# Optimization experiments

Hardware: AMD Instinct MI355X
Metric: run time of the kernel (lower is better)

## Reference

```python
import jax, jax.numpy as jnp
import numpy as np

D_MODEL, D_STATE, D_CONV, EXPAND, HEADDIM = 256, 16, 4, 2, 16
D_INNER = EXPAND * D_MODEL            # 512
NHEADS = D_INNER // HEADDIM           # 32
CONV_DIM = D_INNER + 2 * D_STATE      # 544 (ngroups=1)
D_IN_PROJ = 2 * D_INNER + 2 * D_STATE + NHEADS  # 1088
BATCH, SEQLEN = 8, 4096


def setup_inputs() -> dict:
    key = jax.random.key(0)
    ks = jax.random.split(key, 8)
    u = jax.random.normal(ks[0], (BATCH, SEQLEN, D_MODEL), jnp.float32)
    W_in = jax.random.normal(ks[1], (D_MODEL, D_IN_PROJ), jnp.float32) * 0.02
    conv_w = jax.random.normal(ks[2], (CONV_DIM, 1, D_CONV), jnp.float32) * 0.2
    conv_b = jnp.zeros((CONV_DIM,), jnp.float32)
    # dt_bias init: inverse-softplus of dt ~ Uniform in log-space [dt_min, dt_max]
    dt = jnp.exp(jax.random.uniform(ks[3], (NHEADS,), jnp.float32)
                 * (np.log(0.1) - np.log(0.001)) + np.log(0.001))
    dt = jnp.clip(dt, 1e-4, None)
    dt_bias = dt + jnp.log(-jnp.expm1(-dt))
    A_log = jnp.log(jax.random.uniform(ks[4], (NHEADS,), jnp.float32, 1.0, 16.0))
    D = jnp.ones((NHEADS,), jnp.float32)
    norm_w = jnp.ones((D_INNER,), jnp.float32)
    W_out = jax.random.normal(ks[5], (D_INNER, D_MODEL), jnp.float32) * 0.02
    return dict(u=u, W_in=W_in, conv_w=conv_w, conv_b=conv_b, dt_bias=dt_bias,
                A_log=A_log, D=D, norm_w=norm_w, W_out=W_out)


def _mamba2_forward(u, W_in, conv_w, conv_b, dt_bias, A_log, D, norm_w, W_out):
    batch, seqlen, _ = u.shape
    zxbcdt = u @ W_in                                   # (B, L, 2*d_inner + 2*N + H)
    z = zxbcdt[..., :D_INNER]                           # gate
    xBC = zxbcdt[..., D_INNER:2 * D_INNER + 2 * D_STATE]
    dt = jax.nn.softplus(zxbcdt[..., -NHEADS:] + dt_bias)  # (B, L, H)
    # causal depthwise conv1d over time + SiLU
    xc = jnp.transpose(xBC, (0, 2, 1))                  # (B, C, L)
    xc = jax.lax.conv_general_dilated(
        xc, conv_w, window_strides=(1,), padding=[(D_CONV - 1, 0)],
        feature_group_count=CONV_DIM, dimension_numbers=('NCH', 'OIH', 'NCH'))
    xBC = jax.nn.silu(jnp.transpose(xc, (0, 2, 1)) + conv_b)
    x = xBC[..., :D_INNER].reshape(batch, seqlen, NHEADS, HEADDIM)  # (B,L,H,P)
    Bm = xBC[..., D_INNER:D_INNER + D_STATE]            # (B, L, N), ngroups=1
    Cm = xBC[..., D_INNER + D_STATE:]                   # (B, L, N)
    A = -jnp.exp(A_log)                                 # (H,)
    dA = jnp.exp(dt * A)                                # (B, L, H) decay per step

    # selective scan: h_t = dA_t * h_{t-1} + dt_t * (B_t outer x_t); y_t = C_t . h_t
    def step(h, inp):
        da_t, dt_t, b_t, x_t, c_t = inp
        h = da_t[:, :, None, None] * h + jnp.einsum('bh,bn,bhp->bhpn', dt_t, b_t, x_t)
        y_t = jnp.einsum('bhpn,bn->bhp', h, c_t)
        return h, y_t

    h0 = jnp.zeros((batch, NHEADS, HEADDIM, D_STATE), u.dtype)
    xs = (jnp.moveaxis(dA, 1, 0), jnp.moveaxis(dt, 1, 0),
          jnp.moveaxis(Bm, 1, 0), jnp.moveaxis(x, 1, 0), jnp.moveaxis(Cm, 1, 0))
    _, ys = jax.lax.scan(step, h0, xs)                  # ys: (L, B, H, P)
    y = jnp.moveaxis(ys, 0, 1) + D[None, None, :, None] * x
    y = y.reshape(batch, seqlen, D_INNER)
    # gated RMSNorm (norm_before_gate=False): normalize(y * silu(z)) * weight
    t = y * jax.nn.silu(z)
    t = t * jax.lax.rsqrt(jnp.mean(t * t, axis=-1, keepdims=True) + 1e-5) * norm_w
    return t @ W_out


def reference(u, W_in, conv_w, conv_b, dt_bias, A_log, D, norm_w, W_out):
    return _mamba2_forward(u, W_in, conv_w, conv_b, dt_bias, A_log, D, norm_w, W_out)
```

## Files before the change

### kernel.cpp

```cpp
#include <hip/hip_runtime.h>
#include <hip/hip_bf16.h>
#include <math.h>

#define BATCH   8
#define SEQLEN  4096
#define DMODEL  256
#define DSTATE  16
#define NHEADS  32
#define HEADDIM 16
#define DINNER  512
#define CONVDIM 544
#define DINPROJ 1088
#define NROWS   (BATCH*SEQLEN)
#define CHUNK   64
#define NCH     (SEQLEN/CHUNK)

typedef __attribute__((ext_vector_type(8))) short short8;
typedef __attribute__((ext_vector_type(8))) unsigned short ushort8;
typedef __attribute__((ext_vector_type(4))) float f32x4;

#define LDSP(x) ((__attribute__((address_space(3))) void*)(x))
#define GLBP(x) ((const __attribute__((address_space(1))) void*)(x))

__device__ __forceinline__ float bfu2f(unsigned short u){
  union { float f; unsigned int i; } x; x.i = ((unsigned int)u) << 16; return x.f;
}
__device__ __forceinline__ unsigned short f2bfu(float f){
  union { float f; unsigned int u; } v; v.f = f;
  v.u += 0x7fffu + ((v.u >> 16) & 1u);
  return (unsigned short)(v.u >> 16);
}

__global__ __launch_bounds__(256) void k_cast_u(const float* __restrict__ u, unsigned short* __restrict__ ub){
  int i = blockIdx.x*256 + threadIdx.x;
  float4 v = reinterpret_cast<const float4*>(u)[i];
  ushort4 o; o.x=f2bfu(v.x); o.y=f2bfu(v.y); o.z=f2bfu(v.z); o.w=f2bfu(v.w);
  reinterpret_cast<ushort4*>(ub)[i] = o;
}

__global__ __launch_bounds__(256) void k_transpose_cast(const float* __restrict__ W, unsigned short* __restrict__ WT, int K, int N){
  int idx = blockIdx.x*256 + threadIdx.x;
  if (idx >= N*K) return;
  int n = idx / K, k = idx - n*K;
  WT[idx] = f2bfu(W[(size_t)k*N + n]);
}

template<int EPI, int BN>
__global__ __launch_bounds__(256) void k_gemm(
    const unsigned short* __restrict__ A,
    const unsigned short* __restrict__ BT,
    int K, int nbase,
    unsigned short* __restrict__ oz,
    unsigned short* __restrict__ oxbc,
    float* __restrict__ odtraw,
    float* __restrict__ of32, int Nout)
{
  constexpr int ABYTES = 128*64;
  constexpr int BBYTES = BN*64;
  constexpr int BUFB   = ABYTES + BBYTES;
  constexpr int NF     = BN/32;
  constexpr int BCALLS = BBYTES/4096;
  __shared__ __align__(16) unsigned char lds[2*BUFB];
  const int tid = threadIdx.x;
  const int l   = tid & 63;
  const int w   = tid >> 6;
  const int wr  = w >> 1, wc = w & 1;
  const int bm0 = blockIdx.x * 128;
  const int bn0 = nbase + blockIdx.y * BN;
  const int fr  = l & 15, kq = l >> 4;
  f32x4 acc[4][NF] = {};

  auto STAGE = [&](int buf, int kt){
    const int k0 = kt << 5;
    unsigned char* lb = (unsigned char*)lds + buf*BUFB;
    #pragma unroll
    for (int i = 0; i < 2; ++i){
      int row = w*32 + i*16 + (l>>2);
      int sl  = (l&3) ^ ((row>>1)&3);
      const unsigned short* gp = A + (size_t)(bm0+row)*K + k0 + sl*8;
      __builtin_amdgcn_global_load_lds(GLBP(gp), LDSP(lb + w*2048 + i*1024), 16, 0, 0);
    }
    #pragma unroll
    for (int i = 0; i < BCALLS; ++i){
      int row = w*(BCALLS*16) + i*16 + (l>>2);
      int sl  = (l&3) ^ ((row>>1)&3);
      const unsigned short* gp = BT + (size_t)(bn0+row)*K + k0 + sl*8;
      __builtin_amdgcn_global_load_lds(GLBP(gp), LDSP(lb + ABYTES + w*(BCALLS*1024) + i*1024), 16, 0, 0);
    }
  };

  const int nK = K >> 5;
  STAGE(0, 0);
  __syncthreads();
  int cur = 0;
  for (int kt = 0; kt < nK; ++kt){
    if (kt + 1 < nK) STAGE(cur^1, kt+1);
    const unsigned char* ab = (const unsigned char*)lds + cur*BUFB;
    const unsigned char* bb = ab + ABYTES;
    short8 bf[NF];
    #pragma unroll
    for (int nf = 0; nf < NF; ++nf){
      int rb = wc*(BN/2) + nf*16 + fr;
      bf[nf] = *reinterpret_cast<const short8*>(bb + rb*64 + ((kq ^ ((rb>>1)&3))*16));
    }
    #pragma unroll
    for (int mf = 0; mf < 4; ++mf){
      int ra = wr*64 + mf*16 + fr;
      short8 af = *reinterpret_cast<const short8*>(ab + ra*64 + ((kq ^ ((ra>>1)&3))*16));
      #pragma unroll
      for (int nf = 0; nf < NF; ++nf)
        acc[mf][nf] = __builtin_amdgcn_mfma_f32_16x16x32_bf16(af, bf[nf], acc[mf][nf], 0, 0, 0);
    }
    __syncthreads();
    cur ^= 1;
  }
  #pragma unroll
  for (int mf = 0; mf < 4; ++mf){
    #pragma unroll
    for (int nf = 0; nf < NF; ++nf){
      #pragma unroll
      for (int r = 0; r < 4; ++r){
        int m = bm0 + wr*64 + mf*16 + kq*4 + r;
        int n = bn0 + wc*(BN/2) + nf*16 + fr;
        float v = acc[mf][nf][r];
        if (EPI == 1){
          if (n < DINNER)                 oz[(size_t)m*DINNER + n] = f2bfu(v);
          else if (n < DINNER + CONVDIM)  oxbc[(size_t)m*CONVDIM + (n - DINNER)] = f2bfu(v);
          else                            odtraw[(size_t)m*NHEADS + (n - DINNER - CONVDIM)] = v;
        } else {
          of32[(size_t)m*Nout + n] = v;
        }
      }
    }
  }
}

__global__ __launch_bounds__(256) void k_convbc(const unsigned short* __restrict__ xbc,
                                                const float* __restrict__ cw,
                                                const float* __restrict__ cb,
                                                float* __restrict__ bco){
  const int tid = threadIdx.x;
  const int j = tid & 31;
  const int rt = tid >> 5;
  const int r0 = blockIdx.x*64 + rt*8;
  const int ch = 512 + j;
  const int tloc = r0 & (SEQLEN-1);
  float wv0 = cw[ch*4+0], wv1 = cw[ch*4+1], wv2 = cw[ch*4+2], wv3 = cw[ch*4+3];
  const float bias = cb[ch];
  float xr[11];
  #pragma unroll
  for (int k = 0; k < 11; ++k){
    int r = r0 - 3 + k;
    xr[k] = (tloc - 3 + k < 0) ? 0.f : bfu2f(xbc[(size_t)r*CONVDIM + ch]);
  }
  #pragma unroll
  for (int i = 0; i < 8; ++i){
    float acc = fmaf(wv0, xr[i], fmaf(wv1, xr[i+1], fmaf(wv2, xr[i+2], fmaf(wv3, xr[i+3], bias))));
    bco[(size_t)(r0+i)*32 + j] = acc / (1.f + __expf(-acc));
  }
}

__global__ __launch_bounds__(256) void k_dtda(const float* __restrict__ dtraw,
                                              const float* __restrict__ dt_bias,
                                              const float* __restrict__ A_log,
                                              float* __restrict__ dt_o,
                                              float* __restrict__ dA_o){
  int i = blockIdx.x*256 + threadIdx.x;
  int h = i & (NHEADS-1);
  float x = dtraw[i] + dt_bias[h];
  float dt = (x > 20.f) ? x : log1pf(expf(x));
  dt_o[i] = dt;
  dA_o[i] = expf(-expf(A_log[h]) * dt);
}

__global__ __launch_bounds__(256,4) void k_scan1(
    const unsigned short* __restrict__ xbc, const float* __restrict__ bc,
    const float* __restrict__ dta, const float* __restrict__ daa,
    const float* __restrict__ cwv, const float* __restrict__ cbv,
    const float* __restrict__ Dv,
    float* __restrict__ yl, float* __restrict__ st, float* __restrict__ Pp)
{
  __shared__ float sBC[65*32];
  __shared__ float sdt[65*16];
  __shared__ float sda[65*16];
  const int tid = threadIdx.x;
  const int bid = blockIdx.x;
  const int qh = bid & 1;
  const int c  = (bid >> 1) & (NCH-1);
  const int b  = bid >> 7;
  const int w  = tid >> 6;
  const int l  = tid & 63;
  const int q  = qh*4 + w;
  const int hh = l >> 4, p = l & 15;
  const int h  = q*4 + hh;
  const size_t row0 = (size_t)b*SEQLEN + (size_t)c*CHUNK;
  const int xoff = q*64 + l;
  {
    const float* src = bc + row0*32;
    #pragma unroll
    for (int i = 0; i < 2; ++i){
      int idx = tid + i*256;
      *reinterpret_cast<float4*>(&sBC[idx*4]) = *reinterpret_cast<const float4*>(src + (size_t)idx*4);
    }
  }
  {
    int t = tid >> 2, g = (tid & 3)*4;
    *reinterpret_cast<float4*>(&sdt[t*16+g]) =
      *reinterpret_cast<const float4*>(dta + (row0+t)*NHEADS + qh*16 + g);
    *reinterpret_cast<float4*>(&sda[t*16+g]) =
      *reinterpret_cast<const float4*>(daa + (row0+t)*NHEADS + qh*16 + g);
  }
  const float cw0 = cwv[xoff*4+0], cw1 = cwv[xoff*4+1], cw2 = cwv[xoff*4+2], cw3 = cwv[xoff*4+3];
  const float cb0 = cbv[xoff];
  const float Dh = Dv[h];
  const int dIdx = w*4 + hh;
  float wA, wB, wC;
  if (c == 0){ wA = wB = wC = 0.f; }
  else {
    wA = bfu2f(xbc[(row0-3)*CONVDIM + xoff]);
    wB = bfu2f(xbc[(row0-2)*CONVDIM + xoff]);
    wC = bfu2f(xbc[(row0-1)*CONVDIM + xoff]);
  }
  float xq0 = bfu2f(xbc[(row0+0)*CONVDIM + xoff]);
  float xq1 = bfu2f(xbc[(row0+1)*CONVDIM + xoff]);
  float xq2 = bfu2f(xbc[(row0+2)*CONVDIM + xoff]);
  float xq3 = bfu2f(xbc[(row0+3)*CONVDIM + xoff]);
  __syncthreads();
  float BA[32], BB[32];
  #pragma unroll
  for (int k = 0; k < 8; ++k)
    *reinterpret_cast<float4*>(&BA[4*k]) = *reinterpret_cast<const float4*>(&sBC[4*k]);
  float dtA = sdt[dIdx], daA = sda[dIdx];
  float dtB, daB;
  float hs[16];
  #pragma unroll
  for (int n = 0; n < 16; ++n) hs[n] = 0.f;
  float cum = 1.f;

#define S1STEP(CUR, NXT, DTC, DAC, DTN, DAN, XQ, T) {                          \
    const int t_ = (T);                                                        \
    _Pragma("unroll")                                                          \
    for (int k = 0; k < 8; ++k)                                                \
      *reinterpret_cast<float4*>(&NXT[4*k]) =                                  \
        *reinterpret_cast<const float4*>(&sBC[(t_+1)*32 + 4*k]);               \
    DTN = sdt[(t_+1)*16 + dIdx]; DAN = sda[(t_+1)*16 + dIdx];                  \
    float xnew = bfu2f(xbc[(row0 + t_ + 4)*CONVDIM + xoff]);                   \
    float xc = fmaf(cw0, wA, fmaf(cw1, wB, fmaf(cw2, wC, fmaf(cw3, XQ, cb0))));\
    wA = wB; wB = wC; wC = XQ; XQ = xnew;                                      \
    float xs = xc / (1.f + __expf(-xc));                                       \
    float dx = DTC * xs;                                                       \
    float y_ = 0.f;                                                            \
    _Pragma("unroll")                                                          \
    for (int n = 0; n < 16; ++n) hs[n] = fmaf(DAC, hs[n], dx*CUR[n]);          \
    _Pragma("unroll")                                                          \
    for (int n = 0; n < 16; ++n) y_ = fmaf(hs[n], CUR[16+n], y_);              \
    cum *= DAC;                                                                \
    yl[(row0 + t_)*DINNER + xoff] = y_ + Dh*xs;                                \
  }

  for (int T = 0; T < CHUNK; T += 4){
    S1STEP(BA, BB, dtA, daA, dtB, daB, xq0, T+0);
    S1STEP(BB, BA, dtB, daB, dtA, daA, xq1, T+1);
    S1STEP(BA, BB, dtA, daA, dtB, daB, xq2, T+2);
    S1STEP(BB, BA, dtB, daB, dtA, daA, xq3, T+3);
  }
#undef S1STEP
  float* sp = st + (((size_t)(b*NHEADS + h)*NCH + c)*16 + p)*16;
  #pragma unroll
  for (int k = 0; k < 4; ++k)
    *reinterpret_cast<float4*>(sp + 4*k) = make_float4(hs[4*k], hs[4*k+1], hs[4*k+2], hs[4*k+3]);
  if (p == 0) Pp[((size_t)b*NHEADS + h)*NCH + c] = cum;
}

__global__ __launch_bounds__(64) void k_scan2(float* __restrict__ st, const float* __restrict__ Pp){
  const int bh = blockIdx.x;
  const int l = threadIdx.x;
  float* sb = st + (size_t)bh*NCH*256 + l*4;
  const float* pb = Pp + (size_t)bh*NCH;
  float4 carry = make_float4(0.f,0.f,0.f,0.f);
  float4 Hb[4]; float Pb[4];
  #pragma unroll
  for (int i = 0; i < 4; ++i){
    Hb[i] = *reinterpret_cast<const float4*>(sb + (size_t)i*256);
    Pb[i] = pb[i];
  }
  for (int c0 = 0; c0 < NCH; c0 += 4){
    #pragma unroll
    for (int i = 0; i < 4; ++i){
      const int cc = c0 + i;
      float4 Hc = Hb[i]; float Pc = Pb[i];
      if (cc + 4 < NCH){
        Hb[i] = *reinterpret_cast<const float4*>(sb + (size_t)(cc+4)*256);
        Pb[i] = pb[cc+4];
      }
      *reinterpret_cast<float4*>(sb + (size_t)cc*256) = carry;
      carry.x = fmaf(Pc, carry.x, Hc.x);
      carry.y = fmaf(Pc, carry.y, Hc.y);
      carry.z = fmaf(Pc, carry.z, Hc.z);
      carry.w = fmaf(Pc, carry.w, Hc.w);
    }
  }
}

__global__ __launch_bounds__(256,4) void k_scan3(
    const float* __restrict__ yl, const float* __restrict__ bc,
    const float* __restrict__ daa, const float* __restrict__ st,
    unsigned short* __restrict__ ybf)
{
  __shared__ float sC[65*16];
  __shared__ float sda[65*16];
  const int tid = threadIdx.x;
  const int bid = blockIdx.x;
  const int qh = bid & 1;
  const int c  = (bid >> 1) & (NCH-1);
  const int b  = bid >> 7;
  const int w  = tid >> 6;
  const int l  = tid & 63;
  const int q  = qh*4 + w;
  const int hh = l >> 4, p = l & 15;
  const int h  = q*4 + hh;
  const size_t row0 = (size_t)b*SEQLEN + (size_t)c*CHUNK;
  const int xoff = q*64 + l;
  {
    int t = tid >> 2, g = (tid & 3)*4;
    *reinterpret_cast<float4*>(&sC[t*16+g]) =
      *reinterpret_cast<const float4*>(bc + (row0+t)*32 + 16 + g);
    *reinterpret_cast<float4*>(&sda[t*16+g]) =
      *reinterpret_cast<const float4*>(daa + (row0+t)*NHEADS + qh*16 + g);
  }
  float hi[16];
  {
    const float* sp = st + (((size_t)(b*NHEADS + h)*NCH + c)*16 + p)*16;
    #pragma unroll
    for (int k = 0; k < 4; ++k){
      float4 v = *reinterpret_cast<const float4*>(sp + 4*k);
      hi[4*k] = v.x; hi[4*k+1] = v.y; hi[4*k+2] = v.z; hi[4*k+3] = v.w;
    }
  }
  float yq0 = yl[(row0+0)*DINNER + xoff];
  float yq1 = yl[(row0+1)*DINNER + xoff];
  float yq2 = yl[(row0+2)*DINNER + xoff];
  float yq3 = yl[(row0+3)*DINNER + xoff];
  __syncthreads();
  const int dIdx = w*4 + hh;
  float CA[16], CB[16];
  #pragma unroll
  for (int k = 0; k < 4; ++k)
    *reinterpret_cast<float4*>(&CA[4*k]) = *reinterpret_cast<const float4*>(&sC[4*k]);
  float daA = sda[dIdx], daB;
  float cum = 1.f;

#define S3STEP(CUR, NXT, DAC, DAN, YQ, T) {                                    \
    const int t_ = (T);                                                        \
    _Pragma("unroll")                                                          \
    for (int k = 0; k < 4; ++k)                                                \
      *reinterpret_cast<float4*>(&NXT[4*k]) =                                  \
        *reinterpret_cast<const float4*>(&sC[(t_+1)*16 + 4*k]);                \
    DAN = sda[(t_+1)*16 + dIdx];                                               \
    float ynew = yl[(row0 + t_ + 4)*DINNER + xoff];                            \
    cum *= DAC;                                                                \
    float corr = 0.f;                                                          \
    _Pragma("unroll")                                                          \
    for (int n = 0; n < 16; ++n) corr = fmaf(hi[n], CUR[n], corr);             \
    ybf[(row0 + t_)*DINNER + xoff] = f2bfu(YQ + cum*corr);                     \
    YQ = ynew;                                                                 \
  }

  for (int T = 0; T < CHUNK; T += 4){
    S3STEP(CA, CB, daA, daB, yq0, T+0);
    S3STEP(CB, CA, daB, daA, yq1, T+1);
    S3STEP(CA, CB, daA, daB, yq2, T+2);
    S3STEP(CB, CA, daB, daA, yq3, T+3);
  }
#undef S3STEP
}

__global__ __launch_bounds__(256) void k_gate(const unsigned short* __restrict__ ybf,
                                              unsigned short* __restrict__ zbf,
                                              const float* __restrict__ nw){
  int row = blockIdx.x*4 + (threadIdx.x >> 6);
  int l = threadIdx.x & 63;
  size_t base = (size_t)row*DINNER + l*8;
  ushort8 yv = *reinterpret_cast<const ushort8*>(ybf + base);
  ushort8 zv = *reinterpret_cast<const ushort8*>(zbf + base);
  float tv[8]; float ss = 0.f;
  #pragma unroll
  for (int j = 0; j < 8; ++j){
    float yf = bfu2f(yv[j]);
    float zf = bfu2f(zv[j]);
    float s = zf / (1.f + __expf(-zf));
    float t = yf * s; tv[j] = t; ss += t*t;
  }
  #pragma unroll
  for (int m = 1; m <= 32; m <<= 1) ss += __shfl_xor(ss, m, 64);
  float scale = rsqrtf(ss * (1.f/DINNER) + 1e-5f);
  ushort8 o;
  #pragma unroll
  for (int j = 0; j < 8; ++j) o[j] = f2bfu(tv[j] * scale * nw[l*8+j]);
  *reinterpret_cast<ushort8*>(zbf + base) = o;
}

extern "C" void kernel_launch(void* const* d_in, const int* in_sizes, int n_in,
                              void* d_out, int out_size, void* d_ws, size_t ws_size,
                              hipStream_t stream)
{
  const float* u       = (const float*)d_in[0];
  const float* W_in    = (const float*)d_in[1];
  const float* conv_w  = (const float*)d_in[2];
  const float* conv_b  = (const float*)d_in[3];
  const float* dt_bias = (const float*)d_in[4];
  const float* A_log   = (const float*)d_in[5];
  const float* Dvec    = (const float*)d_in[6];
  const float* norm_w  = (const float*)d_in[7];
  const float* W_out   = (const float*)d_in[8];
  float* out = (float*)d_out;
  char* ws = (char*)d_ws;

  unsigned short* ubf   = (unsigned short*)(ws + 0);
  float* chst           = (float*)(ws + 0);
  unsigned short* wintT = (unsigned short*)(ws + 16777216);
  unsigned short* woutT = (unsigned short*)(ws + 17334272);
  unsigned short* zbf   = (unsigned short*)(ws + 17596416);
  unsigned short* xbcbf = (unsigned short*)(ws + 51150848);
  float* dtraw          = (float*)(ws + 86802432);
  float* Pp             = dtraw;
  float* ylocal         = (float*)(ws + 90996736);
  float* convoBC        = (float*)(ws + 158105600);
  float* dtq            = (float*)(ws + 162299904);
  float* daq            = (float*)(ws + 166494208);
  unsigned short* ybf   = xbcbf;

  k_cast_u<<<NROWS*DMODEL/1024, 256, 0, stream>>>(u, ubf);
  k_transpose_cast<<<(DINPROJ*DMODEL+255)/256, 256, 0, stream>>>(W_in, wintT, DMODEL, DINPROJ);
  k_transpose_cast<<<(DINNER*DMODEL+255)/256, 256, 0, stream>>>(W_out, woutT, DINNER, DMODEL);

  dim3 g1a(NROWS/128, 1024/128);
  k_gemm<1,128><<<g1a, 256, 0, stream>>>(ubf, wintT, DMODEL, 0, zbf, xbcbf, dtraw, nullptr, 0);
  dim3 g1b(NROWS/128, 1);
  k_gemm<1,64><<<g1b, 256, 0, stream>>>(ubf, wintT, DMODEL, 1024, zbf, xbcbf, dtraw, nullptr, 0);

  k_convbc<<<NROWS/64, 256, 0, stream>>>(xbcbf, conv_w, conv_b, convoBC);
  k_dtda<<<NROWS*NHEADS/256, 256, 0, stream>>>(dtraw, dt_bias, A_log, dtq, daq);

  k_scan1<<<BATCH*2*NCH, 256, 0, stream>>>(xbcbf, convoBC, dtq, daq, conv_w, conv_b, Dvec,
                                           ylocal, chst, Pp);
  k_scan2<<<BATCH*NHEADS, 64, 0, stream>>>(chst, Pp);
  k_scan3<<<BATCH*2*NCH, 256, 0, stream>>>(ylocal, convoBC, daq, chst, ybf);

  k_gate<<<NROWS/4, 256, 0, stream>>>(ybf, zbf, norm_w);

  dim3 g2(NROWS/128, DMODEL/128);
  k_gemm<2,128><<<g2, 256, 0, stream>>>(zbf, woutT, DINNER, 0, nullptr, nullptr, nullptr, out, DMODEL);
}
```

Measured before the change: 177.0 us.

## Replace LDS-staged GEMM with direct global-to-register MFMA operand loads

The GEMM kernel drops its double-buffered LDS staging (global_load_lds plus swizzled LDS reads and per-iteration barriers). Each wave now loads its bf16 A and B fragments straight from global memory into registers, and K becomes a template parameter so the loop can be unrolled. This removes the LDS traffic and __syncthreads cost, since K is small (256/512). In exchange, operands shared across waves are re-read from global/L2 with no reuse, and the strided 16-byte row loads may coalesce poorly.

```diff
diff --git a/kernel.cpp b/kernel.cpp
--- a/kernel.cpp
+++ b/kernel.cpp
@@ -19,9 +19,6 @@
 typedef __attribute__((ext_vector_type(8))) unsigned short ushort8;
 typedef __attribute__((ext_vector_type(4))) float f32x4;
 
-#define LDSP(x) ((__attribute__((address_space(3))) void*)(x))
-#define GLBP(x) ((const __attribute__((address_space(1))) void*)(x))
-
 __device__ __forceinline__ float bfu2f(unsigned short u){
   union { float f; unsigned int i; } x; x.i = ((unsigned int)u) << 16; return x.f;
 }
@@ -45,22 +42,17 @@
   WT[idx] = f2bfu(W[(size_t)k*N + n]);
 }
 
-template<int EPI, int BN>
+template<int EPI, int BN, int K>
 __global__ __launch_bounds__(256) void k_gemm(
     const unsigned short* __restrict__ A,
     const unsigned short* __restrict__ BT,
-    int K, int nbase,
+    int nbase,
     unsigned short* __restrict__ oz,
     unsigned short* __restrict__ oxbc,
     float* __restrict__ odtraw,
     float* __restrict__ of32, int Nout)
 {
-  constexpr int ABYTES = 128*64;
-  constexpr int BBYTES = BN*64;
-  constexpr int BUFB   = ABYTES + BBYTES;
-  constexpr int NF     = BN/32;
-  constexpr int BCALLS = BBYTES/4096;
-  __shared__ __align__(16) unsigned char lds[2*BUFB];
+  constexpr int NF = BN/32;
   const int tid = threadIdx.x;
   const int l   = tid & 63;
   const int w   = tid >> 6;
@@ -69,50 +61,23 @@
   const int bn0 = nbase + blockIdx.y * BN;
   const int fr  = l & 15, kq = l >> 4;
   f32x4 acc[4][NF] = {};
-
-  auto STAGE = [&](int buf, int kt){
-    const int k0 = kt << 5;
-    unsigned char* lb = (unsigned char*)lds + buf*BUFB;
-    #pragma unroll
-    for (int i = 0; i < 2; ++i){
-      int row = w*32 + i*16 + (l>>2);
-      int sl  = (l&3) ^ ((row>>1)&3);
-      const unsigned short* gp = A + (size_t)(bm0+row)*K + k0 + sl*8;
-      __builtin_amdgcn_global_load_lds(GLBP(gp), LDSP(lb + w*2048 + i*1024), 16, 0, 0);
-    }
-    #pragma unroll
-    for (int i = 0; i < BCALLS; ++i){
-      int row = w*(BCALLS*16) + i*16 + (l>>2);
-      int sl  = (l&3) ^ ((row>>1)&3);
-      const unsigned short* gp = BT + (size_t)(bn0+row)*K + k0 + sl*8;
-      __builtin_amdgcn_global_load_lds(GLBP(gp), LDSP(lb + ABYTES + w*(BCALLS*1024) + i*1024), 16, 0, 0);
-    }
-  };
-
-  const int nK = K >> 5;
-  STAGE(0, 0);
-  __syncthreads();
-  int cur = 0;
-  for (int kt = 0; kt < nK; ++kt){
-    if (kt + 1 < nK) STAGE(cur^1, kt+1);
-    const unsigned char* ab = (const unsigned char*)lds + cur*BUFB;
-    const unsigned char* bb = ab + ABYTES;
-    short8 bf[NF];
-    #pragma unroll
-    for (int nf = 0; nf < NF; ++nf){
-      int rb = wc*(BN/2) + nf*16 + fr;
-      bf[nf] = *reinterpret_cast<const short8*>(bb + rb*64 + ((kq ^ ((rb>>1)&3))*16));
-    }
+  const unsigned short* Ap = A  + (size_t)(bm0 + wr*64 + fr)*K + kq*8;
+  const unsigned short* Bp = BT + (size_t)(bn0 + wc*(BN/2) + fr)*K + kq*8;
+  #pragma unroll 2
+  for (int kt = 0; kt < K/32; ++kt){
+    short8 af[4], bf[NF];
+    #pragma unroll
+    for (int mf = 0; mf < 4; ++mf)
+      af[mf] = *reinterpret_cast<const short8*>(Ap + (size_t)mf*16*K + kt*32);
+    #pragma unroll
+    for (int nf = 0; nf < NF; ++nf)
+      bf[nf] = *reinterpret_cast<const short8*>(Bp + (size_t)nf*16*K + kt*32);
     #pragma unroll
     for (int mf = 0; mf < 4; ++mf){
-      int ra = wr*64 + mf*16 + fr;
-      short8 af = *reinterpret_cast<const short8*>(ab + ra*64 + ((kq ^ ((ra>>1)&3))*16));
       #pragma unroll
       for (int nf = 0; nf < NF; ++nf)
-        acc[mf][nf] = __builtin_amdgcn_mfma_f32_16x16x32_bf16(af, bf[nf], acc[mf][nf], 0, 0, 0);
+        acc[mf][nf] = __builtin_amdgcn_mfma_f32_16x16x32_bf16(af[mf], bf[nf], acc[mf][nf], 0, 0, 0);
     }
-    __syncthreads();
-    cur ^= 1;
   }
   #pragma unroll
   for (int mf = 0; mf < 4; ++mf){
@@ -435,9 +400,9 @@
   k_transpose_cast<<<(DINNER*DMODEL+255)/256, 256, 0, stream>>>(W_out, woutT, DINNER, DMODEL);
 
   dim3 g1a(NROWS/128, 1024/128);
-  k_gemm<1,128><<<g1a, 256, 0, stream>>>(ubf, wintT, DMODEL, 0, zbf, xbcbf, dtraw, nullptr, 0);
+  k_gemm<1,128,DMODEL><<<g1a, 256, 0, stream>>>(ubf, wintT, 0, zbf, xbcbf, dtraw, nullptr, 0);
   dim3 g1b(NROWS/128, 1);
-  k_gemm<1,64><<<g1b, 256, 0, stream>>>(ubf, wintT, DMODEL, 1024, zbf, xbcbf, dtraw, nullptr, 0);
+  k_gemm<1,64,DMODEL><<<g1b, 256, 0, stream>>>(ubf, wintT, 1024, zbf, xbcbf, dtraw, nullptr, 0);
 
   k_convbc<<<NROWS/64, 256, 0, stream>>>(xbcbf, conv_w, conv_b, convoBC);
   k_dtda<<<NROWS*NHEADS/256, 256, 0, stream>>>(dtraw, dt_bias, A_log, dtq, daq);
@@ -449,6 +414,6 @@
 
   k_gate<<<NROWS/4, 256, 0, stream>>>(ybf, zbf, norm_w);
 
-  dim3 g2(NROWS/128, DMODEL/128);
-  k_gemm<2,128><<<g2, 256, 0, stream>>>(zbf, woutT, DINNER, 0, nullptr, nullptr, nullptr, out, DMODEL);
-}
+  dim3 g2(NROWS/128, 2);
+  k_gemm<2,128,DINNER><<<g2, 256, 0, stream>>>(zbf, woutT, 0, nullptr, nullptr, nullptr, out, DMODEL);
+}
```

Result: slower. 234.6 us (+32.5%).
